# Optimization experiments

Measured on AMD Instinct MI355X. Metric: run time of the kernel, lower is better.

## Reference

```python
import jax, jax.numpy as jnp
import numpy as np

NEG_BIG = -1e10  # K.switch(A==0, -1e10, 0) mask value
LRELU_ALPHA = 0.2


def setup_inputs() -> dict:
    key = jax.random.key(0)
    kX, kA, kW, kS, kN = jax.random.split(key, 5)
    B, N, F, H, F_ = 4, 2048, 256, 8, 64
    X = jax.random.normal(kX, (B, N, F), dtype=jnp.float32)
    A = jax.random.bernoulli(kA, 0.05, (B, N, N)).astype(jnp.float32)
    eye = jnp.eye(N, dtype=jnp.float32)[None]
    A = jnp.maximum(A, eye)
    W = jax.random.normal(kW, (H, F, F_), dtype=jnp.float32) * 0.05
    a_self = jax.random.normal(kS, (H, F_), dtype=jnp.float32) * 0.05
    a_neigh = jax.random.normal(kN, (H, F_), dtype=jnp.float32) * 0.05
    return {"X": X, "A": A, "W": W, "a_self": a_self, "a_neigh": a_neigh}


def reference(X, A, W, a_self, a_neigh):
    # per-head linear transform, vectorized over heads: [B,H,N,F_]
    h = jnp.einsum('bnf,hfo->bhno', X, W)
    att_s = jnp.einsum('bhno,ho->bhn', h, a_self)    # attn_for_self
    att_n = jnp.einsum('bhno,ho->bhn', h, a_neigh)   # attn_for_neighs
    # broadcast-add -> dense NxN scores per head, LeakyReLU(0.2)
    dense = att_s[:, :, :, None] + att_n[:, :, None, :]          # [B,H,N,N]
    dense = jax.nn.leaky_relu(dense, LRELU_ALPHA)
    mask = jnp.where(A == 0.0, NEG_BIG, 0.0)[:, None, :, :]      # [B,1,N,N]
    attn = jax.nn.softmax(dense + mask, axis=-1)
    # weighted aggregation (dropout is identity at inference / attn_dropout=0)
    out = jnp.einsum('bhnm,bhmo->bhno', attn, h)                 # [B,H,N,F_]
    out = jax.nn.relu(out)                                       # per-head activation (concat mode)
    B, H, N, F_ = out.shape
    return out.transpose(0, 2, 1, 3).reshape(B, N, H * F_)       # concat heads
```

## Files before the change

### kernel.cpp

```cpp
#include <hip/hip_runtime.h>


constexpr int GN  = 2048;
constexpr int GHF = 512;

using sh8    = __attribute__((ext_vector_type(8))) short;
using us4g   = __attribute__((ext_vector_type(4))) unsigned short;
using f32x4g = __attribute__((ext_vector_type(4))) float;
using u32x4g = __attribute__((ext_vector_type(4))) unsigned int;
using i32x4g = __attribute__((ext_vector_type(4))) int;

__device__ inline float gat_bf2f(unsigned short u) {
    union { unsigned int i; float f; } c; c.i = ((unsigned int)u) << 16; return c.f;
}
__device__ inline unsigned short gat_f2bf(float f) {
    union { float f; unsigned int i; } c; c.f = f;
    return (unsigned short)((c.i + 0x7fffu + ((c.i >> 16) & 1u)) >> 16);
}
__device__ inline int gat_isf32(const float* __restrict__ Aw) {
    float a = Aw[0];
    return (a == 0.0f) || (a == 1.0f);
}
__device__ inline unsigned int gat_enc(float f) {
    union { float f; unsigned int u; } c; c.f = f;
    return (c.u & 0x80000000u) ? ~c.u : (c.u | 0x80000000u);
}
__device__ inline float gat_dec(unsigned int e) {
    union { float f; unsigned int u; } c;
    c.u = (e & 0x80000000u) ? (e & 0x7fffffffu) : ~e;
    return c.f;
}
__device__ inline size_t gat_hswz_idx(int o, int j) {
    int jc = j >> 5, quad = (j >> 3) & 3, e = j & 7;
    int lane = quad * 16 + (o & 15);
    return (((size_t)(jc * 4 + (o >> 4))) * 64 + lane) * 8 + e;
}

__global__ void GraphAttention_62981400429165_kernel() {}

constexpr size_t OFF_HS   = 256;
constexpr size_t OFF_ATTS = OFF_HS   + 8388608;
constexpr size_t OFF_TB   = OFF_ATTS + 262144;
constexpr size_t OFF_MASK = OFF_TB   + 262144;
constexpr size_t OFF_MAXN = OFF_MASK + 2097152;
constexpr size_t OFF_XC   = OFF_MAXN + 256;
constexpr size_t OFF_WC   = OFF_XC   + 4194304;

__global__ __launch_bounds__(256) void k_mask_conv(const void* __restrict__ Araw,
                                                   const void* __restrict__ Xraw,
                                                   const void* __restrict__ Wraw,
                                                   unsigned long long* __restrict__ mask,
                                                   unsigned int* __restrict__ maxn_enc,
                                                   unsigned short* __restrict__ Xc,
                                                   unsigned short* __restrict__ Wc) {
    int tid = threadIdx.x, blk = blockIdx.x;
    int isf = gat_isf32((const float*)Araw);
    if (blk < 65536) {
        if (blk == 0 && tid < 32) maxn_enc[tid] = 0u;
        size_t idx = (size_t)blk * 256 + tid;
        int nz;
        if (isf) nz = (((const float*)Araw)[idx] != 0.0f);
        else     nz = (((const unsigned short*)Araw)[idx] != 0);
        unsigned long long bal = __ballot(nz);
        if ((tid & 63) == 0) mask[idx >> 6] = bal;
    } else if (blk < 73728) {
        int i = (blk - 65536) * 256 + tid;
        Xc[i] = isf ? gat_f2bf(((const float*)Xraw)[i]) : ((const unsigned short*)Xraw)[i];
    } else {
        int i = (blk - 73728) * 256 + tid;
        Wc[i] = isf ? gat_f2bf(((const float*)Wraw)[i]) : ((const unsigned short*)Wraw)[i];
    }
}

constexpr int LDW = 264;
__global__ __launch_bounds__(256) void k_gemm1(const unsigned short* __restrict__ Xc,
                                               const unsigned short* __restrict__ Wc,
                                               const void* __restrict__ aSraw,
                                               const void* __restrict__ aNraw,
                                               const float* __restrict__ Aw,
                                               unsigned short* __restrict__ hswz,
                                               float* __restrict__ att_s,
                                               unsigned int* __restrict__ Tb,
                                               unsigned int* __restrict__ maxn_enc) {
    int blk = blockIdx.x;
    int bh = blk >> 3, it = blk & 7;
    int b = bh >> 3, hh = bh & 7;
    int isf = gat_isf32(Aw);
    __shared__ unsigned short Wt[64 * LDW];
    for (int idx = threadIdx.x; idx < 256 * 64; idx += 256) {
        int k = idx >> 6, col = idx & 63;
        Wt[col * LDW + k] = Wc[(hh * 256 + k) * 64 + col];
    }
    __syncthreads();
#if defined(__gfx950__)
    int wave = threadIdx.x >> 6, lane = threadIdx.x & 63;
    int lrw = lane & 15, quad = lane >> 4;
    int row0 = it * 256 + wave * 64;
    f32x4g acc[4][4] = {};
    for (int k0 = 0; k0 < 256; k0 += 32) {
        sh8 a[4], w[4];
        for (int rt = 0; rt < 4; rt++)
            a[rt] = *(const sh8*)&Xc[((size_t)(b * GN) + row0 + rt * 16 + lrw) * 256 + k0 + quad * 8];
        for (int ct = 0; ct < 4; ct++)
            w[ct] = *(const sh8*)&Wt[(ct * 16 + lrw) * LDW + k0 + quad * 8];
        for (int rt = 0; rt < 4; rt++)
            for (int ct = 0; ct < 4; ct++)
                acc[rt][ct] = __builtin_amdgcn_mfma_f32_16x16x32_bf16(a[rt], w[ct], acc[rt][ct], 0, 0, 0);
    }
    float as_l[4], an_l[4];
    for (int ct = 0; ct < 4; ct++) {
        int col = hh * 64 + ct * 16 + lrw;
        as_l[ct] = isf ? ((const float*)aSraw)[col] : gat_bf2f(((const unsigned short*)aSraw)[col]);
        an_l[ct] = isf ? ((const float*)aNraw)[col] : gat_bf2f(((const unsigned short*)aNraw)[col]);
    }
    float wmax = -3e38f;
    for (int rt = 0; rt < 4; rt++)
        for (int r = 0; r < 4; r++) {
            float ps = acc[rt][0][r] * as_l[0] + acc[rt][1][r] * as_l[1]
                     + acc[rt][2][r] * as_l[2] + acc[rt][3][r] * as_l[3];
            float pn = acc[rt][0][r] * an_l[0] + acc[rt][1][r] * an_l[1]
                     + acc[rt][2][r] * an_l[2] + acc[rt][3][r] * an_l[3];
            for (int off = 1; off < 16; off <<= 1) {
                ps += __shfl_xor(ps, off);
                pn += __shfl_xor(pn, off);
            }
            int row = row0 + rt * 16 + quad * 4 + r;
            if (lrw == 0) {
                att_s[bh * GN + row] = ps;
                Tb[bh * GN + row] = ((unsigned int)gat_f2bf(__expf(pn)) << 16)
                                  | (unsigned int)gat_f2bf(__expf(0.2f * pn));
            }
            wmax = fmaxf(wmax, pn);
        }
    wmax = fmaxf(wmax, __shfl_xor(wmax, 16));
    wmax = fmaxf(wmax, __shfl_xor(wmax, 32));
    if (lane == 0) atomicMax(&maxn_enc[bh], gat_enc(wmax));
    __syncthreads();
    unsigned short* CtT = Wt;
    for (int rt = 0; rt < 4; rt++)
        for (int ct = 0; ct < 4; ct++) {
            int o = ct * 16 + lrw;
            int nloc = wave * 64 + rt * 16 + quad * 4;
            us4g v;
            v[0] = gat_f2bf(acc[rt][ct][0]);
            v[1] = gat_f2bf(acc[rt][ct][1]);
            v[2] = gat_f2bf(acc[rt][ct][2]);
            v[3] = gat_f2bf(acc[rt][ct][3]);
            *(us4g*)&CtT[o * LDW + nloc] = v;
        }
    __syncthreads();
    for (int k = 0; k < 8; k++) {
        int id = k * 256 + threadIdx.x;
        int ln = id & 63, t = id >> 6;
        int jc_loc = t >> 2, ct = t & 3;
        int lrw2 = ln & 15, quad2 = ln >> 4;
        int o = ct * 16 + lrw2;
        int nloc = jc_loc * 32 + quad2 * 8;
        sh8 v = *(const sh8*)&CtT[o * LDW + nloc];
        size_t dst = ((((size_t)(bh * 64 + it * 8 + jc_loc)) * 4 + ct) * 64 + ln) * 8;
        *(sh8*)&hswz[dst] = v;
    }
#else
    int row = it * 256 + threadIdx.x;
    float hrow[64];
    for (int col = 0; col < 64; col++) {
        float s = 0.f;
        for (int k = 0; k < 256; k++)
            s += gat_bf2f(Xc[((size_t)(b * GN) + row) * 256 + k]) * gat_bf2f(Wt[col * LDW + k]);
        hrow[col] = s;
        hswz[(size_t)bh * 64 * GN * 2 / 2 * 0 + 0] = hswz[0];
    }
    for (int col = 0; col < 64; col++) {
        size_t base = (size_t)bh * 64 * GN;
        hswz[base + gat_hswz_idx(col, row)] = gat_f2bf(hrow[col]);
    }
    float ps = 0.f, pn = 0.f;
    for (int col = 0; col < 64; col++) {
        float as = isf ? ((const float*)aSraw)[hh * 64 + col] : gat_bf2f(((const unsigned short*)aSraw)[hh * 64 + col]);
        float an = isf ? ((const float*)aNraw)[hh * 64 + col] : gat_bf2f(((const unsigned short*)aNraw)[hh * 64 + col]);
        ps += hrow[col] * as;
        pn += hrow[col] * an;
    }
    att_s[bh * GN + row] = ps;
    Tb[bh * GN + row] = ((unsigned int)gat_f2bf(__expf(pn)) << 16)
                      | (unsigned int)gat_f2bf(__expf(0.2f * pn));
    atomicMax(&maxn_enc[bh], gat_enc(pn));
#endif
}

__global__ __launch_bounds__(128, 4) void k_attn_av(const unsigned int* __restrict__ mask32,
                                                    const unsigned short* __restrict__ hswz,
                                                    const float* __restrict__ att_s,
                                                    const unsigned int* __restrict__ Tb,
                                                    const unsigned int* __restrict__ maxn_enc,
                                                    const float* __restrict__ Aw,
                                                    void* __restrict__ outv) {
    int blk = blockIdx.x;
    int bh = blk & 31, it = blk >> 5;
    int b = bh >> 3, hh = bh & 7;
    int i0 = it * 32;
    int tid = threadIdx.x;
    int isf = gat_isf32(Aw);
    float maxn = gat_dec(maxn_enc[bh]);
    const unsigned int* Tp = Tb + (size_t)bh * GN;
#if defined(__gfx950__)
    int wave = tid >> 6, lane = tid & 63, lrw = lane & 15, quad = lane >> 4;
    int kq = quad * 8;
    int j0 = wave * 1024;
    const unsigned short* hs = hswz + ((size_t)(bh * 64) + wave * 32) * 2048 + lane * 8;
    float k1[2], k2[2], T0[2];
    const unsigned int* mrf[2];
    for (int f = 0; f < 2; f++) {
        int row = i0 + f * 16 + lrw;
        float s = att_s[bh * GN + row];
        float z = s + maxn;
        float c = fmaxf(z, 0.2f * z);
        k1[f] = __expf(s - c);
        k2[f] = __expf(0.2f * s - c);
        T0[f] = __expf(-s);
        mrf[f] = mask32 + ((size_t)(b * GN) + row) * 64 + wave * 32;
    }
    f32x4g acc[2][4] = {};
    f32x4g accl[2] = {};
    sh8 ones;
#pragma unroll
    for (int e = 0; e < 8; e++) ones[e] = (short)0x3f80;

#pragma unroll 1
    for (int jg = 0; jg < 8; jg++) {
        u32x4g m0 = *(const u32x4g*)&mrf[0][jg * 4];
        u32x4g m1 = *(const u32x4g*)&mrf[1][jg * 4];
#pragma unroll
        for (int sj = 0; sj < 4; sj++) {
            int jc = jg * 4 + sj;
            int jq = j0 + jc * 32 + kq;
            u32x4g tA = *(const u32x4g*)&Tp[jq];
            u32x4g tB = *(const u32x4g*)&Tp[jq + 4];
            const unsigned short* hp = hs + jc * 2048;
            sh8 b0 = *(const sh8*)&hp[0];
            sh8 b1 = *(const sh8*)&hp[512];
            sh8 b2 = *(const sh8*)&hp[1024];
            sh8 b3 = *(const sh8*)&hp[1536];
            unsigned int w0 = m0[sj] >> kq;
            unsigned int w1 = m1[sj] >> kq;
            unsigned int q0[8], q1[8];
#pragma unroll
            for (int e = 0; e < 8; e++) {
                unsigned int word = (e < 4) ? tA[e] : tB[e - 4];
                float Ev  = __uint_as_float(word & 0xffff0000u);
                float E5v = __uint_as_float(word << 16);
                float p0 = (Ev > T0[0]) ? (k1[0] * Ev) : (k2[0] * E5v);
                float p1 = (Ev > T0[1]) ? (k1[1] * Ev) : (k2[1] * E5v);
                p0 = ((w0 >> e) & 1u) ? p0 : 0.0f;
                p1 = ((w1 >> e) & 1u) ? p1 : 0.0f;
                q0[e] = __float_as_uint(p0);
                q1[e] = __float_as_uint(p1);
            }
            i32x4g f0, f1;
#pragma unroll
            for (int pp = 0; pp < 4; pp++) {
                f0[pp] = (int)((q0[2 * pp] >> 16) | (q0[2 * pp + 1] & 0xffff0000u));
                f1[pp] = (int)((q1[2 * pp] >> 16) | (q1[2 * pp + 1] & 0xffff0000u));
            }
            sh8 af0 = *(sh8*)&f0;
            sh8 af1 = *(sh8*)&f1;
            acc[0][0] = __builtin_amdgcn_mfma_f32_16x16x32_bf16(af0, b0, acc[0][0], 0, 0, 0);
            acc[1][0] = __builtin_amdgcn_mfma_f32_16x16x32_bf16(af1, b0, acc[1][0], 0, 0, 0);
            acc[0][1] = __builtin_amdgcn_mfma_f32_16x16x32_bf16(af0, b1, acc[0][1], 0, 0, 0);
            acc[1][1] = __builtin_amdgcn_mfma_f32_16x16x32_bf16(af1, b1, acc[1][1], 0, 0, 0);
            acc[0][2] = __builtin_amdgcn_mfma_f32_16x16x32_bf16(af0, b2, acc[0][2], 0, 0, 0);
            acc[1][2] = __builtin_amdgcn_mfma_f32_16x16x32_bf16(af1, b2, acc[1][2], 0, 0, 0);
            acc[0][3] = __builtin_amdgcn_mfma_f32_16x16x32_bf16(af0, b3, acc[0][3], 0, 0, 0);
            acc[1][3] = __builtin_amdgcn_mfma_f32_16x16x32_bf16(af1, b3, acc[1][3], 0, 0, 0);
            accl[0] = __builtin_amdgcn_mfma_f32_16x16x32_bf16(af0, ones, accl[0], 0, 0, 0);
            accl[1] = __builtin_amdgcn_mfma_f32_16x16x32_bf16(af1, ones, accl[1], 0, 0, 0);
        }
    }
    __shared__ float lred[2 * 32];
    __shared__ float lsum[32];
    __shared__ float red[2 * 2 * 16 * 17];
    if (lrw == 0) {
#pragma unroll
        for (int f = 0; f < 2; f++)
#pragma unroll
            for (int r = 0; r < 4; r++)
                lred[wave * 32 + f * 16 + quad * 4 + r] = accl[f][r];
    }
    __syncthreads();
    if (tid < 32)
        lsum[tid] = 1.0f / (lred[tid] + lred[32 + tid]);
    __syncthreads();
    for (int ct = 0; ct < 4; ct++) {
#pragma unroll
        for (int f = 0; f < 2; f++)
#pragma unroll
            for (int r = 0; r < 4; r++)
                red[wave * 544 + f * 272 + (quad * 4 + r) * 17 + lrw] = acc[f][ct][r];
        __syncthreads();
#pragma unroll
        for (int k = 0; k < 4; k++) {
            int pos = k * 128 + tid;
            int f = pos >> 8, r16 = (pos >> 4) & 15, c16 = pos & 15;
            int bse = f * 272 + r16 * 17 + c16;
            float sum = red[bse] + red[bse + 544];
            float v = sum * lsum[f * 16 + r16];
            v = v > 0.f ? v : 0.f;
            int row = i0 + f * 16 + r16;
            size_t o = ((size_t)(b * GN) + row) * GHF + hh * 64 + ct * 16 + c16;
            if (isf) ((float*)outv)[o] = v;
            else     ((unsigned short*)outv)[o] = gat_f2bf(v);
        }
        __syncthreads();
    }
#else
    int row = i0 + (tid >> 2), chh = (tid & 3) * 16;
    const unsigned short* hbb = hswz + (size_t)(bh * 64) * GN;
    const unsigned int* mr = mask32 + ((size_t)(b * GN) + row) * 64;
    float s = att_s[bh * GN + row];
    float z = s + maxn;
    float c = fmaxf(z, 0.2f * z);
    float k1 = __expf(s - c), k2 = __expf(0.2f * s - c), T0 = __expf(-s);
    float l = 0.f;
    float accS[16] = {};
    for (int j = 0; j < GN; j++) {
        if (!((mr[j >> 5] >> (j & 31)) & 1u)) continue;
        unsigned int word = Tp[j];
        float Ev  = __uint_as_float(word & 0xffff0000u);
        float E5v = __uint_as_float(word << 16);
        float p = (Ev > T0) ? (k1 * Ev) : (k2 * E5v);
        union { float f; unsigned int u; } t; t.f = p; t.u &= 0xffff0000u;
        l += t.f;
        for (int cc = 0; cc < 16; cc++)
            accS[cc] += t.f * gat_bf2f(hbb[gat_hswz_idx(chh + cc, j)]);
    }
    float li = 1.0f / l;
    for (int cc = 0; cc < 16; cc++) {
        float v = accS[cc] * li; v = v > 0.f ? v : 0.f;
        size_t oi = ((size_t)(b * GN) + row) * GHF + hh * 64 + chh + cc;
        if (isf) ((float*)outv)[oi] = v;
        else     ((unsigned short*)outv)[oi] = gat_f2bf(v);
    }
#endif
}

extern "C" void kernel_launch(void* const* d_in, const int* in_sizes, int n_in,
                              void* d_out, int out_size, void* d_ws, size_t ws_size,
                              hipStream_t stream) {
    const void* X  = d_in[0];
    const void* A  = d_in[1];
    const void* W  = d_in[2];
    const void* aS = d_in[3];
    const void* aN = d_in[4];

    char* ws = (char*)d_ws;
    unsigned short* hswz = (unsigned short*)(ws + OFF_HS);
    float* att_s = (float*)(ws + OFF_ATTS);
    unsigned int* Tb = (unsigned int*)(ws + OFF_TB);
    unsigned long long* mask = (unsigned long long*)(ws + OFF_MASK);
    unsigned int* maxn_enc = (unsigned int*)(ws + OFF_MAXN);
    unsigned short* Xc = (unsigned short*)(ws + OFF_XC);
    unsigned short* Wc = (unsigned short*)(ws + OFF_WC);

    k_mask_conv<<<74240, 256, 0, stream>>>(A, X, W, mask, maxn_enc, Xc, Wc);
    k_gemm1<<<256, 256, 0, stream>>>(Xc, Wc, aS, aN, (const float*)A,
                                     hswz, att_s, Tb, maxn_enc);
    k_attn_av<<<2048, 128, 0, stream>>>((const unsigned int*)mask, hswz,
                                        att_s, Tb, maxn_enc,
                                        (const float*)A, d_out);
}
```

Measured before the change: 201.3 us.

## Vectorize preprocessing, shrink GEMM tiles, widen attention blocks, simplify softmax select

The mask/convert kernel now has each thread handle 8 elements with vector loads, writing one mask byte per thread. The GEMM kernel uses 64-row tiles (1024 blocks) with vectorized W staging to raise occupancy. The attention kernel splits the key range over 4 waves of 256 threads instead of 2, replaces the threshold select with fmaxf and sbfe masking, and packs bf16 with v_cvt_pk_bf16_f32. Together these cut memory-bound preprocessing cost and raise parallelism, at the price of more cross-wave reduction in shared memory and a change from truncation to rounding when converting attention weights to bf16.

```diff
diff --git a/kernel.cpp b/kernel.cpp
--- a/kernel.cpp
+++ b/kernel.cpp
@@ -55,20 +55,53 @@
                                                    unsigned short* __restrict__ Wc) {
     int tid = threadIdx.x, blk = blockIdx.x;
     int isf = gat_isf32((const float*)Araw);
-    if (blk < 65536) {
+    if (blk < 8192) {
         if (blk == 0 && tid < 32) maxn_enc[tid] = 0u;
-        size_t idx = (size_t)blk * 256 + tid;
-        int nz;
-        if (isf) nz = (((const float*)Araw)[idx] != 0.0f);
-        else     nz = (((const unsigned short*)Araw)[idx] != 0);
-        unsigned long long bal = __ballot(nz);
-        if ((tid & 63) == 0) mask[idx >> 6] = bal;
-    } else if (blk < 73728) {
-        int i = (blk - 65536) * 256 + tid;
-        Xc[i] = isf ? gat_f2bf(((const float*)Xraw)[i]) : ((const unsigned short*)Xraw)[i];
+        size_t i8 = ((size_t)blk * 256 + tid) * 8;
+        unsigned int byte = 0;
+        if (isf) {
+            f32x4g v0 = *(const f32x4g*)((const float*)Araw + i8);
+            f32x4g v1 = *(const f32x4g*)((const float*)Araw + i8 + 4);
+#pragma unroll
+            for (int e = 0; e < 4; e++) {
+                byte |= (v0[e] != 0.0f ? 1u : 0u) << e;
+                byte |= (v1[e] != 0.0f ? 1u : 0u) << (e + 4);
+            }
+        } else {
+            u32x4g v = *(const u32x4g*)((const unsigned short*)Araw + i8);
+#pragma unroll
+            for (int w = 0; w < 4; w++) {
+                byte |= ((v[w] & 0xffffu) != 0u ? 1u : 0u) << (2 * w);
+                byte |= ((v[w] >> 16) != 0u ? 1u : 0u) << (2 * w + 1);
+            }
+        }
+        ((unsigned char*)mask)[i8 >> 3] = (unsigned char)byte;
+    } else if (blk < 9216) {
+        size_t i8 = ((size_t)(blk - 8192) * 256 + tid) * 8;
+        if (isf) {
+            f32x4g v0 = *(const f32x4g*)((const float*)Xraw + i8);
+            f32x4g v1 = *(const f32x4g*)((const float*)Xraw + i8 + 4);
+            us4g lo, hi;
+#pragma unroll
+            for (int e = 0; e < 4; e++) { lo[e] = gat_f2bf(v0[e]); hi[e] = gat_f2bf(v1[e]); }
+            *(us4g*)&Xc[i8]     = lo;
+            *(us4g*)&Xc[i8 + 4] = hi;
+        } else {
+            *(u32x4g*)&Xc[i8] = *(const u32x4g*)((const unsigned short*)Xraw + i8);
+        }
     } else {
-        int i = (blk - 73728) * 256 + tid;
-        Wc[i] = isf ? gat_f2bf(((const float*)Wraw)[i]) : ((const unsigned short*)Wraw)[i];
+        size_t i8 = ((size_t)(blk - 9216) * 256 + tid) * 8;
+        if (isf) {
+            f32x4g v0 = *(const f32x4g*)((const float*)Wraw + i8);
+            f32x4g v1 = *(const f32x4g*)((const float*)Wraw + i8 + 4);
+            us4g lo, hi;
+#pragma unroll
+            for (int e = 0; e < 4; e++) { lo[e] = gat_f2bf(v0[e]); hi[e] = gat_f2bf(v1[e]); }
+            *(us4g*)&Wc[i8]     = lo;
+            *(us4g*)&Wc[i8 + 4] = hi;
+        } else {
+            *(u32x4g*)&Wc[i8] = *(const u32x4g*)((const unsigned short*)Wraw + i8);
+        }
     }
 }
 
@@ -83,73 +116,81 @@
                                                unsigned int* __restrict__ Tb,
                                                unsigned int* __restrict__ maxn_enc) {
     int blk = blockIdx.x;
-    int bh = blk >> 3, it = blk & 7;
+    int bh = blk >> 5, it = blk & 31;
     int b = bh >> 3, hh = bh & 7;
     int isf = gat_isf32(Aw);
     __shared__ unsigned short Wt[64 * LDW];
-    for (int idx = threadIdx.x; idx < 256 * 64; idx += 256) {
-        int k = idx >> 6, col = idx & 63;
-        Wt[col * LDW + k] = Wc[(hh * 256 + k) * 64 + col];
+    {
+        int cg = threadIdx.x & 7, kb = threadIdx.x >> 3;
+        for (int kk = 0; kk < 256; kk += 32) {
+            int k = kk + kb;
+            sh8 v = *(const sh8*)&Wc[((size_t)hh * 256 + k) * 64 + cg * 8];
+#pragma unroll
+            for (int e = 0; e < 8; e++)
+                Wt[(cg * 8 + e) * LDW + k] = (unsigned short)v[e];
+        }
     }
     __syncthreads();
 #if defined(__gfx950__)
     int wave = threadIdx.x >> 6, lane = threadIdx.x & 63;
     int lrw = lane & 15, quad = lane >> 4;
-    int row0 = it * 256 + wave * 64;
-    f32x4g acc[4][4] = {};
+    int row0 = it * 64 + wave * 16;
+    f32x4g acc[4] = {};
     for (int k0 = 0; k0 < 256; k0 += 32) {
-        sh8 a[4], w[4];
-        for (int rt = 0; rt < 4; rt++)
-            a[rt] = *(const sh8*)&Xc[((size_t)(b * GN) + row0 + rt * 16 + lrw) * 256 + k0 + quad * 8];
+        sh8 a = *(const sh8*)&Xc[((size_t)(b * GN) + row0 + lrw) * 256 + k0 + quad * 8];
+        sh8 w[4];
+#pragma unroll
         for (int ct = 0; ct < 4; ct++)
             w[ct] = *(const sh8*)&Wt[(ct * 16 + lrw) * LDW + k0 + quad * 8];
-        for (int rt = 0; rt < 4; rt++)
-            for (int ct = 0; ct < 4; ct++)
-                acc[rt][ct] = __builtin_amdgcn_mfma_f32_16x16x32_bf16(a[rt], w[ct], acc[rt][ct], 0, 0, 0);
+#pragma unroll
+        for (int ct = 0; ct < 4; ct++)
+            acc[ct] = __builtin_amdgcn_mfma_f32_16x16x32_bf16(a, w[ct], acc[ct], 0, 0, 0);
     }
     float as_l[4], an_l[4];
+#pragma unroll
     for (int ct = 0; ct < 4; ct++) {
         int col = hh * 64 + ct * 16 + lrw;
         as_l[ct] = isf ? ((const float*)aSraw)[col] : gat_bf2f(((const unsigned short*)aSraw)[col]);
         an_l[ct] = isf ? ((const float*)aNraw)[col] : gat_bf2f(((const unsigned short*)aNraw)[col]);
     }
     float wmax = -3e38f;
-    for (int rt = 0; rt < 4; rt++)
-        for (int r = 0; r < 4; r++) {
-            float ps = acc[rt][0][r] * as_l[0] + acc[rt][1][r] * as_l[1]
-                     + acc[rt][2][r] * as_l[2] + acc[rt][3][r] * as_l[3];
-            float pn = acc[rt][0][r] * an_l[0] + acc[rt][1][r] * an_l[1]
-                     + acc[rt][2][r] * an_l[2] + acc[rt][3][r] * an_l[3];
-            for (int off = 1; off < 16; off <<= 1) {
-                ps += __shfl_xor(ps, off);
-                pn += __shfl_xor(pn, off);
-            }
-            int row = row0 + rt * 16 + quad * 4 + r;
-            if (lrw == 0) {
-                att_s[bh * GN + row] = ps;
-                Tb[bh * GN + row] = ((unsigned int)gat_f2bf(__expf(pn)) << 16)
-                                  | (unsigned int)gat_f2bf(__expf(0.2f * pn));
-            }
-            wmax = fmaxf(wmax, pn);
-        }
+#pragma unroll
+    for (int r = 0; r < 4; r++) {
+        float ps = acc[0][r] * as_l[0] + acc[1][r] * as_l[1]
+                 + acc[2][r] * as_l[2] + acc[3][r] * as_l[3];
+        float pn = acc[0][r] * an_l[0] + acc[1][r] * an_l[1]
+                 + acc[2][r] * an_l[2] + acc[3][r] * an_l[3];
+        for (int off = 1; off < 16; off <<= 1) {
+            ps += __shfl_xor(ps, off);
+            pn += __shfl_xor(pn, off);
+        }
+        int row = row0 + quad * 4 + r;
+        if (lrw == 0) {
+            att_s[bh * GN + row] = ps;
+            Tb[bh * GN + row] = ((unsigned int)gat_f2bf(__expf(pn)) << 16)
+                              | (unsigned int)gat_f2bf(__expf(0.2f * pn));
+        }
+        wmax = fmaxf(wmax, pn);
+    }
     wmax = fmaxf(wmax, __shfl_xor(wmax, 16));
     wmax = fmaxf(wmax, __shfl_xor(wmax, 32));
     if (lane == 0) atomicMax(&maxn_enc[bh], gat_enc(wmax));
     __syncthreads();
     unsigned short* CtT = Wt;
-    for (int rt = 0; rt < 4; rt++)
-        for (int ct = 0; ct < 4; ct++) {
-            int o = ct * 16 + lrw;
-            int nloc = wave * 64 + rt * 16 + quad * 4;
-            us4g v;
-            v[0] = gat_f2bf(acc[rt][ct][0]);
-            v[1] = gat_f2bf(acc[rt][ct][1]);
-            v[2] = gat_f2bf(acc[rt][ct][2]);
-            v[3] = gat_f2bf(acc[rt][ct][3]);
-            *(us4g*)&CtT[o * LDW + nloc] = v;
-        }
+#pragma unroll
+    for (int ct = 0; ct < 4; ct++) {
+        int o = ct * 16 + lrw;
+        int nloc = wave * 16 + quad * 4;
+        us4g v;
+        v[0] = gat_f2bf(acc[ct][0]);
+        v[1] = gat_f2bf(acc[ct][1]);
+        v[2] = gat_f2bf(acc[ct][2]);
+        v[3] = gat_f2bf(acc[ct][3]);
+        *(us4g*)&CtT[o * LDW + nloc] = v;
+    }
     __syncthreads();
-    for (int k = 0; k < 8; k++) {
+#pragma unroll
+    for (int k = 0; k < 2; k++) {
         int id = k * 256 + threadIdx.x;
         int ln = id & 63, t = id >> 6;
         int jc_loc = t >> 2, ct = t & 3;
@@ -157,38 +198,38 @@
         int o = ct * 16 + lrw2;
         int nloc = jc_loc * 32 + quad2 * 8;
         sh8 v = *(const sh8*)&CtT[o * LDW + nloc];
-        size_t dst = ((((size_t)(bh * 64 + it * 8 + jc_loc)) * 4 + ct) * 64 + ln) * 8;
+        size_t dst = ((((size_t)(bh * 64 + it * 2 + jc_loc)) * 4 + ct) * 64 + ln) * 8;
         *(sh8*)&hswz[dst] = v;
     }
 #else
-    int row = it * 256 + threadIdx.x;
-    float hrow[64];
-    for (int col = 0; col < 64; col++) {
-        float s = 0.f;
-        for (int k = 0; k < 256; k++)
-            s += gat_bf2f(Xc[((size_t)(b * GN) + row) * 256 + k]) * gat_bf2f(Wt[col * LDW + k]);
-        hrow[col] = s;
-        hswz[(size_t)bh * 64 * GN * 2 / 2 * 0 + 0] = hswz[0];
-    }
-    for (int col = 0; col < 64; col++) {
+    if (threadIdx.x < 64) {
+        int row = it * 64 + threadIdx.x;
+        float hrow[64];
+        for (int col = 0; col < 64; col++) {
+            float sacc = 0.f;
+            for (int k = 0; k < 256; k++)
+                sacc += gat_bf2f(Xc[((size_t)(b * GN) + row) * 256 + k]) * gat_bf2f(Wt[col * LDW + k]);
+            hrow[col] = sacc;
+        }
         size_t base = (size_t)bh * 64 * GN;
-        hswz[base + gat_hswz_idx(col, row)] = gat_f2bf(hrow[col]);
-    }
-    float ps = 0.f, pn = 0.f;
-    for (int col = 0; col < 64; col++) {
-        float as = isf ? ((const float*)aSraw)[hh * 64 + col] : gat_bf2f(((const unsigned short*)aSraw)[hh * 64 + col]);
-        float an = isf ? ((const float*)aNraw)[hh * 64 + col] : gat_bf2f(((const unsigned short*)aNraw)[hh * 64 + col]);
-        ps += hrow[col] * as;
-        pn += hrow[col] * an;
-    }
-    att_s[bh * GN + row] = ps;
-    Tb[bh * GN + row] = ((unsigned int)gat_f2bf(__expf(pn)) << 16)
-                      | (unsigned int)gat_f2bf(__expf(0.2f * pn));
-    atomicMax(&maxn_enc[bh], gat_enc(pn));
+        for (int col = 0; col < 64; col++)
+            hswz[base + gat_hswz_idx(col, row)] = gat_f2bf(hrow[col]);
+        float ps = 0.f, pn = 0.f;
+        for (int col = 0; col < 64; col++) {
+            float as = isf ? ((const float*)aSraw)[hh * 64 + col] : gat_bf2f(((const unsigned short*)aSraw)[hh * 64 + col]);
+            float an = isf ? ((const float*)aNraw)[hh * 64 + col] : gat_bf2f(((const unsigned short*)aNraw)[hh * 64 + col]);
+            ps += hrow[col] * as;
+            pn += hrow[col] * an;
+        }
+        att_s[bh * GN + row] = ps;
+        Tb[bh * GN + row] = ((unsigned int)gat_f2bf(__expf(pn)) << 16)
+                          | (unsigned int)gat_f2bf(__expf(0.2f * pn));
+        atomicMax(&maxn_enc[bh], gat_enc(pn));
+    }
 #endif
 }
 
-__global__ __launch_bounds__(128, 4) void k_attn_av(const unsigned int* __restrict__ mask32,
+__global__ __launch_bounds__(256, 6) void k_attn_av(const unsigned int* __restrict__ mask32,
                                                     const unsigned short* __restrict__ hswz,
                                                     const float* __restrict__ att_s,
                                                     const unsigned int* __restrict__ Tb,
@@ -206,9 +247,9 @@
 #if defined(__gfx950__)
     int wave = tid >> 6, lane = tid & 63, lrw = lane & 15, quad = lane >> 4;
     int kq = quad * 8;
-    int j0 = wave * 1024;
-    const unsigned short* hs = hswz + ((size_t)(bh * 64) + wave * 32) * 2048 + lane * 8;
-    float k1[2], k2[2], T0[2];
+    int j0 = wave * 512;
+    const unsigned short* hs = hswz + ((size_t)(bh * 64) + wave * 16) * 2048 + lane * 8;
+    float k1[2], k2[2];
     const unsigned int* mrf[2];
     for (int f = 0; f < 2; f++) {
         int row = i0 + f * 16 + lrw;
@@ -217,8 +258,7 @@
         float c = fmaxf(z, 0.2f * z);
         k1[f] = __expf(s - c);
         k2[f] = __expf(0.2f * s - c);
-        T0[f] = __expf(-s);
-        mrf[f] = mask32 + ((size_t)(b * GN) + row) * 64 + wave * 32;
+        mrf[f] = mask32 + ((size_t)(b * GN) + row) * 64 + wave * 16;
     }
     f32x4g acc[2][4] = {};
     f32x4g accl[2] = {};
@@ -227,7 +267,7 @@
     for (int e = 0; e < 8; e++) ones[e] = (short)0x3f80;
 
 #pragma unroll 1
-    for (int jg = 0; jg < 8; jg++) {
+    for (int jg = 0; jg < 4; jg++) {
         u32x4g m0 = *(const u32x4g*)&mrf[0][jg * 4];
         u32x4g m1 = *(const u32x4g*)&mrf[1][jg * 4];
 #pragma unroll
@@ -249,18 +289,25 @@
                 unsigned int word = (e < 4) ? tA[e] : tB[e - 4];
                 float Ev  = __uint_as_float(word & 0xffff0000u);
                 float E5v = __uint_as_float(word << 16);
-                float p0 = (Ev > T0[0]) ? (k1[0] * Ev) : (k2[0] * E5v);
-                float p1 = (Ev > T0[1]) ? (k1[1] * Ev) : (k2[1] * E5v);
-                p0 = ((w0 >> e) & 1u) ? p0 : 0.0f;
-                p1 = ((w1 >> e) & 1u) ? p1 : 0.0f;
-                q0[e] = __float_as_uint(p0);
-                q1[e] = __float_as_uint(p1);
+                float p0 = fmaxf(k1[0] * Ev, k2[0] * E5v);
+                float p1 = fmaxf(k1[1] * Ev, k2[1] * E5v);
+                unsigned int s0 = (unsigned int)__builtin_amdgcn_sbfe((int)w0, (unsigned)e, 1u);
+                unsigned int s1 = (unsigned int)__builtin_amdgcn_sbfe((int)w1, (unsigned)e, 1u);
+                q0[e] = __float_as_uint(p0) & s0;
+                q1[e] = __float_as_uint(p1) & s1;
             }
             i32x4g f0, f1;
 #pragma unroll
             for (int pp = 0; pp < 4; pp++) {
-                f0[pp] = (int)((q0[2 * pp] >> 16) | (q0[2 * pp + 1] & 0xffff0000u));
-                f1[pp] = (int)((q1[2 * pp] >> 16) | (q1[2 * pp + 1] & 0xffff0000u));
+                unsigned int r0, r1;
+                asm("v_cvt_pk_bf16_f32 %0, %1, %2"
+                    : "=v"(r0)
+                    : "v"(__uint_as_float(q0[2 * pp])), "v"(__uint_as_float(q0[2 * pp + 1])));
+                asm("v_cvt_pk_bf16_f32 %0, %1, %2"
+                    : "=v"(r1)
+                    : "v"(__uint_as_float(q1[2 * pp])), "v"(__uint_as_float(q1[2 * pp + 1])));
+                f0[pp] = (int)r0;
+                f1[pp] = (int)r1;
             }
             sh8 af0 = *(sh8*)&f0;
             sh8 af1 = *(sh8*)&f1;
@@ -276,9 +323,9 @@
             accl[1] = __builtin_amdgcn_mfma_f32_16x16x32_bf16(af1, ones, accl[1], 0, 0, 0);
         }
     }
-    __shared__ float lred[2 * 32];
+    __shared__ float lred[4 * 32];
     __shared__ float lsum[32];
-    __shared__ float red[2 * 2 * 16 * 17];
+    __shared__ float red[4 * 2 * 16 * 17];
     if (lrw == 0) {
 #pragma unroll
         for (int f = 0; f < 2; f++)
@@ -288,7 +335,7 @@
     }
     __syncthreads();
     if (tid < 32)
-        lsum[tid] = 1.0f / (lred[tid] + lred[32 + tid]);
+        lsum[tid] = 1.0f / (lred[tid] + lred[32 + tid] + lred[64 + tid] + lred[96 + tid]);
     __syncthreads();
     for (int ct = 0; ct < 4; ct++) {
 #pragma unroll
@@ -298,11 +345,11 @@
                 red[wave * 544 + f * 272 + (quad * 4 + r) * 17 + lrw] = acc[f][ct][r];
         __syncthreads();
 #pragma unroll
-        for (int k = 0; k < 4; k++) {
-            int pos = k * 128 + tid;
+        for (int k = 0; k < 2; k++) {
+            int pos = k * 256 + tid;
             int f = pos >> 8, r16 = (pos >> 4) & 15, c16 = pos & 15;
             int bse = f * 272 + r16 * 17 + c16;
-            float sum = red[bse] + red[bse + 544];
+            float sum = red[bse] + red[bse + 544] + red[bse + 1088] + red[bse + 1632];
             float v = sum * lsum[f * 16 + r16];
             v = v > 0.f ? v : 0.f;
             int row = i0 + f * 16 + r16;
@@ -313,28 +360,28 @@
         __syncthreads();
     }
 #else
-    int row = i0 + (tid >> 2), chh = (tid & 3) * 16;
+    int row = i0 + (tid >> 3), chh = (tid & 7) * 8;
     const unsigned short* hbb = hswz + (size_t)(bh * 64) * GN;
     const unsigned int* mr = mask32 + ((size_t)(b * GN) + row) * 64;
     float s = att_s[bh * GN + row];
     float z = s + maxn;
     float c = fmaxf(z, 0.2f * z);
-    float k1 = __expf(s - c), k2 = __expf(0.2f * s - c), T0 = __expf(-s);
+    float k1 = __expf(s - c), k2 = __expf(0.2f * s - c);
     float l = 0.f;
-    float accS[16] = {};
+    float accS[8] = {};
     for (int j = 0; j < GN; j++) {
         if (!((mr[j >> 5] >> (j & 31)) & 1u)) continue;
         unsigned int word = Tp[j];
         float Ev  = __uint_as_float(word & 0xffff0000u);
         float E5v = __uint_as_float(word << 16);
-        float p = (Ev > T0) ? (k1 * Ev) : (k2 * E5v);
+        float p = fmaxf(k1 * Ev, k2 * E5v);
         union { float f; unsigned int u; } t; t.f = p; t.u &= 0xffff0000u;
         l += t.f;
-        for (int cc = 0; cc < 16; cc++)
+        for (int cc = 0; cc < 8; cc++)
             accS[cc] += t.f * gat_bf2f(hbb[gat_hswz_idx(chh + cc, j)]);
     }
     float li = 1.0f / l;
-    for (int cc = 0; cc < 16; cc++) {
+    for (int cc = 0; cc < 8; cc++) {
         float v = accS[cc] * li; v = v > 0.f ? v : 0.f;
         size_t oi = ((size_t)(b * GN) + row) * GHF + hh * 64 + chh + cc;
         if (isf) ((float*)outv)[oi] = v;
@@ -361,10 +408,10 @@
     unsigned short* Xc = (unsigned short*)(ws + OFF_XC);
     unsigned short* Wc = (unsigned short*)(ws + OFF_WC);
 
-    k_mask_conv<<<74240, 256, 0, stream>>>(A, X, W, mask, maxn_enc, Xc, Wc);
-    k_gemm1<<<256, 256, 0, stream>>>(Xc, Wc, aS, aN, (const float*)A,
-                                     hswz, att_s, Tb, maxn_enc);
-    k_attn_av<<<2048, 128, 0, stream>>>((const unsigned int*)mask, hswz,
+    k_mask_conv<<<9280, 256, 0, stream>>>(A, X, W, mask, maxn_enc, Xc, Wc);
+    k_gemm1<<<1024, 256, 0, stream>>>(Xc, Wc, aS, aN, (const float*)A,
+                                      hswz, att_s, Tb, maxn_enc);
+    k_attn_av<<<2048, 256, 0, stream>>>((const unsigned int*)mask, hswz,
                                         att_s, Tb, maxn_enc,
                                         (const float*)A, d_out);
 }
```

Measured after the change: 253.8 us. +26.1%, slower.
